# Optimization experiments

Hardware: AMD Instinct MI355X
Metric: run time of the kernel (lower is better)

Reference implementation:

```python
import jax, jax.numpy as jnp
import numpy as np

B, T, N, D, NH = 4, 12, 512, 512, 8
DH = D // NH
# Faithful quirk of the original: inside cal_attention, d = K.shape[-1] (the HEAD dim = 64)
# and it divides by sqrt(d / n_h) = sqrt(64/8) = sqrt(8), NOT sqrt(64).
SCALE = 1.0 / np.sqrt(DH / NH).astype(np.float32)
NEG = -1000000000.0


def setup_inputs() -> dict:
    key = jax.random.key(0)
    ks = jax.random.split(key, 9)
    s = 1.0 / np.sqrt(D).astype(np.float32)
    return {
        "V": jax.random.normal(ks[0], (B, T, N, D), jnp.float32),
        "K": jax.random.normal(ks[1], (B, T, N, D), jnp.float32),
        "Q": jax.random.normal(ks[2], (B, T, N, D), jnp.float32),
        "M": jax.random.randint(ks[3], (B, T, N, N), 0, 2, jnp.int32),
        "wx_w": jax.random.normal(ks[4], (3 * D, D), jnp.float32) * s,
        "wx_b": jax.random.normal(ks[5], (3 * D,), jnp.float32) * 0.02,
        "wo_w": jax.random.normal(ks[6], (D, D), jnp.float32) * s,
        "wo_b": jax.random.normal(ks[7], (D,), jnp.float32) * 0.02,
    }


def _split_heads(x):
    # [B,T,N,D] -> [B,T,h,N,d_h]
    b, t, n, _ = x.shape
    return x.reshape(b, t, n, NH, DH).transpose(0, 1, 3, 2, 4)


def reference(V, K, Q, M, wx_w, wx_b, wo_w, wo_b):
    # self-attention branch: Q, K, V all come from wx(Q); inputs V/K are ignored
    wx_o = Q @ wx_w.T + wx_b                      # [B,T,N,3D]
    q, k, v = jnp.split(wx_o, 3, axis=-1)
    q, k, v = _split_heads(q), _split_heads(k), _split_heads(v)  # [B,T,h,N,d_h]
    scores = jnp.einsum("bthqd,bthkd->bthqk", q, k) * SCALE      # [B,T,h,N,N]
    scores = scores + M[:, :, None, :, :].astype(scores.dtype) * NEG
    attn = jax.nn.softmax(scores, axis=-1)
    out = jnp.einsum("bthqk,bthkd->bthqd", attn, v)              # [B,T,h,N,d_h]
    out = out.transpose(0, 1, 3, 2, 4).reshape(B, T, N, D)       # concat heads
    return out @ wo_w.T + wo_b
```

## Files before the change

kernel.cpp:

```cpp
#include <hip/hip_runtime.h>
#include <cstdint>
#include <cstddef>

typedef __bf16 bf16x8_t __attribute__((ext_vector_type(8)));
typedef float f32x4_t __attribute__((ext_vector_type(4)));

#define SCALE 0.3535533905932738f
#define LOG2E 1.4426950408889634f
#define NEG -1000000000.0f

__device__ __forceinline__ unsigned short f2b(float f) {
    unsigned int u = __builtin_bit_cast(unsigned int, f);
    u += 0x7FFFu + ((u >> 16) & 1u);
    return (unsigned short)(u >> 16);
}

__device__ __forceinline__ int swz(int row, int chunk) {
    return row * 64 + (((chunk ^ (row & 7)) << 3));
}

__device__ __forceinline__ void gld16(const void* g, void* l) {
    __builtin_amdgcn_global_load_lds(
        (const __attribute__((address_space(1))) unsigned int*)g,
        (__attribute__((address_space(3))) unsigned int*)l,
        16, 0, 0);
}

__device__ __forceinline__ unsigned int cvt_pk_bf16(float lo, float hi) {
    unsigned int r;
    asm("v_cvt_pk_bf16_f32 %0, %1, %2" : "=v"(r) : "v"(lo), "v"(hi));
    return r;
}

__global__ __launch_bounds__(256) void cvt_kernel(const float* __restrict__ in,
                                                  unsigned short* __restrict__ out,
                                                  int n4) {
    int i = blockIdx.x * 256 + threadIdx.x;
    if (i >= n4) return;
    const float4 f = reinterpret_cast<const float4*>(in)[i];
    ushort4 o;
    o.x = f2b(f.x); o.y = f2b(f.y); o.z = f2b(f.z); o.w = f2b(f.w);
    reinterpret_cast<ushort4*>(out)[i] = o;
}

__global__ __launch_bounds__(256) void gemm_qkv(
    const unsigned short* __restrict__ A,
    const unsigned short* __restrict__ W,
    const float* __restrict__ bias,
    unsigned short* __restrict__ qb,
    unsigned short* __restrict__ kb,
    unsigned short* __restrict__ vT)
{
    __shared__ unsigned short As[128*64];
    __shared__ unsigned short Bs[128*64];
    const int tid = threadIdx.x;
    const int lane = tid & 63;
    const int l15 = lane & 15, lhi = lane >> 4;
    const int wid = tid >> 6, wr = wid >> 1, wc = wid & 1;
    const int bid = blockIdx.x;
    const int sid = (bid & 7) * 288 + (bid >> 3);
    const int m0 = (sid / 12) * 128, n0 = (sid % 12) * 128;
    const int rA = lane >> 3;
    const int sc = (lane & 7) ^ rA;

    f32x4_t acc[4][4] = {};

    for (int k0 = 0; k0 < 512; k0 += 64) {
        __syncthreads();
#pragma unroll
        for (int j = 0; j < 4; ++j) {
            const int ch = 4*wid + j;
            const int gr = ch*8 + rA;
            gld16(&A[(size_t)(m0+gr)*512 + k0 + sc*8], &As[ch*512]);
            gld16(&W[(size_t)(n0+gr)*512 + k0 + sc*8], &Bs[ch*512]);
        }
        asm volatile("s_waitcnt vmcnt(0)" ::: "memory");
        __syncthreads();
#pragma unroll
        for (int kk = 0; kk < 2; ++kk) {
            bf16x8_t af[4], bfr[4];
#pragma unroll
            for (int x = 0; x < 4; ++x) {
                af[x]  = *reinterpret_cast<const bf16x8_t*>(&As[swz(wr*64 + x*16 + l15, kk*4 + lhi)]);
                bfr[x] = *reinterpret_cast<const bf16x8_t*>(&Bs[swz(wc*64 + x*16 + l15, kk*4 + lhi)]);
            }
#pragma unroll
            for (int mi = 0; mi < 4; ++mi)
#pragma unroll
                for (int nj = 0; nj < 4; ++nj)
                    acc[mi][nj] = __builtin_amdgcn_mfma_f32_16x16x32_bf16(af[mi], bfr[nj], acc[mi][nj], 0, 0, 0);
        }
    }

#pragma unroll
    for (int mi = 0; mi < 4; ++mi) {
#pragma unroll
        for (int nj = 0; nj < 4; ++nj) {
            const int gn = n0 + wc*64 + nj*16 + l15;
            const float bi = bias[gn];
            const int which = gn >> 9, hh = (gn >> 6) & 7, dh = gn & 63;
#pragma unroll
            for (int i = 0; i < 4; ++i) {
                const int gm = m0 + wr*64 + mi*16 + lhi*4 + i;
                const int bt = gm >> 9, row = gm & 511;
                const float v = acc[mi][nj][i] + bi;
                const size_t ho = (size_t)bt*8 + hh;
                if (which == 0)      qb[ho*(512*64) + (size_t)row*64 + dh] = f2b(v * (SCALE * LOG2E));
                else if (which == 1) kb[ho*(512*64) + (size_t)row*64 + dh] = f2b(v);
                else                 vT[ho*(64*512) + (size_t)dh*512 + row] = f2b(v);
            }
        }
    }
}

__global__ __launch_bounds__(512, 4) void attn_kernel(
    const unsigned short* __restrict__ qb,
    const unsigned short* __restrict__ kb,
    const unsigned short* __restrict__ vT,
    const int* __restrict__ Mm,
    unsigned short* __restrict__ ob)
{
    __shared__ unsigned short Ks[2][64*64];
    __shared__ unsigned short Vs[2][64*64];
    __shared__ unsigned short Ps[8][32*40];

    const int tid = threadIdx.x;
    const int lane = tid & 63;
    const int w = tid >> 6;
    const int l15 = lane & 15, lhi = lane >> 4;
    const int bid = blockIdx.x;
    const int sid = (bid & 7) * 96 + (bid >> 3);
    const int qt = sid & 1;
    const int h  = (sid >> 1) & 7;
    const int bt = sid >> 4;
    const int q0 = qt*256 + w*32;
    const size_t hoQK = ((size_t)bt*8 + h) * (512*64);
    const size_t hoV  = ((size_t)bt*8 + h) * (64*512);

    const int rA = lane >> 3;
    const int sc = (lane & 7) ^ rA;
    const int trK = w*8 + rA;

    bf16x8_t qf[2][2];
#pragma unroll
    for (int qmi = 0; qmi < 2; ++qmi)
#pragma unroll
        for (int kk = 0; kk < 2; ++kk)
            qf[qmi][kk] = *reinterpret_cast<const bf16x8_t*>(
                &qb[hoQK + (size_t)(q0 + qmi*16 + l15)*64 + kk*32 + lhi*8]);

    bf16x8_t ones;
    {
        uint4 u = {0x3F803F80u, 0x3F803F80u, 0x3F803F80u, 0x3F803F80u};
        ones = __builtin_bit_cast(bf16x8_t, u);
    }

    f32x4_t of[2][4] = {};
    f32x4_t ofl[2] = {};

    const size_t mrow0 = ((size_t)bt*512 + q0 + l15) * 512;

    gld16(&kb[hoQK + (size_t)trK*64 + sc*8],          &Ks[0][w*512]);
    gld16(&vT[hoV + (size_t)(w*8 + rA)*512 + sc*8],   &Vs[0][w*512]);

    for (int kbk = 0; kbk < 8; ++kbk) {
        const int cur = kbk & 1;
        if (kbk < 7) {
            const int t = kbk + 1, nb = cur ^ 1;
            gld16(&kb[hoQK + (size_t)(t*64 + trK)*64 + sc*8],        &Ks[nb][w*512]);
            gld16(&vT[hoV + (size_t)(w*8 + rA)*512 + t*64 + sc*8],   &Vs[nb][w*512]);
            asm volatile("s_waitcnt vmcnt(2)" ::: "memory");
        } else {
            asm volatile("s_waitcnt vmcnt(0)" ::: "memory");
        }
        __syncthreads();

        int4 mv[4][2];
#pragma unroll
        for (int knj = 0; knj < 4; ++knj)
#pragma unroll
            for (int qmi = 0; qmi < 2; ++qmi)
                mv[knj][qmi] = *reinterpret_cast<const int4*>(
                    &Mm[mrow0 + (size_t)(qmi*16)*512 + kbk*64 + knj*16 + lhi*4]);

        f32x4_t sa[4][2] = {};
#pragma unroll
        for (int kk = 0; kk < 2; ++kk) {
            bf16x8_t kf[4];
#pragma unroll
            for (int knj = 0; knj < 4; ++knj)
                kf[knj] = *reinterpret_cast<const bf16x8_t*>(&Ks[cur][swz(knj*16 + l15, kk*4 + lhi)]);
#pragma unroll
            for (int knj = 0; knj < 4; ++knj)
#pragma unroll
                for (int qmi = 0; qmi < 2; ++qmi)
                    sa[knj][qmi] = __builtin_amdgcn_mfma_f32_16x16x32_bf16(kf[knj], qf[qmi][kk], sa[knj][qmi], 0, 0, 0);
        }

#pragma unroll
        for (int knj = 0; knj < 4; ++knj)
#pragma unroll
            for (int qmi = 0; qmi < 2; ++qmi) {
                sa[knj][qmi][0] = exp2f(fmaf((float)mv[knj][qmi].x, NEG, sa[knj][qmi][0]));
                sa[knj][qmi][1] = exp2f(fmaf((float)mv[knj][qmi].y, NEG, sa[knj][qmi][1]));
                sa[knj][qmi][2] = exp2f(fmaf((float)mv[knj][qmi].z, NEG, sa[knj][qmi][2]));
                sa[knj][qmi][3] = exp2f(fmaf((float)mv[knj][qmi].w, NEG, sa[knj][qmi][3]));
            }

#pragma unroll
        for (int half = 0; half < 2; ++half) {
#pragma unroll
            for (int qmi = 0; qmi < 2; ++qmi)
#pragma unroll
                for (int knjh = 0; knjh < 2; ++knjh) {
                    const int knj = half*2 + knjh;
                    const unsigned int p01 = cvt_pk_bf16(sa[knj][qmi][0], sa[knj][qmi][1]);
                    const unsigned int p23 = cvt_pk_bf16(sa[knj][qmi][2], sa[knj][qmi][3]);
                    const int base = (qmi*16 + l15)*40 + knjh*16 + lhi*4;
                    *reinterpret_cast<unsigned int*>(&Ps[w][base])     = p01;
                    *reinterpret_cast<unsigned int*>(&Ps[w][base + 2]) = p23;
                }

            bf16x8_t pf[2];
#pragma unroll
            for (int qmi = 0; qmi < 2; ++qmi)
                pf[qmi] = *reinterpret_cast<const bf16x8_t*>(&Ps[w][(qmi*16 + l15)*40 + lhi*8]);

            bf16x8_t vf[4];
#pragma unroll
            for (int dj = 0; dj < 4; ++dj)
                vf[dj] = *reinterpret_cast<const bf16x8_t*>(&Vs[cur][swz(dj*16 + l15, half*4 + lhi)]);

#pragma unroll
            for (int qmi = 0; qmi < 2; ++qmi) {
                ofl[qmi] = __builtin_amdgcn_mfma_f32_16x16x32_bf16(pf[qmi], ones, ofl[qmi], 0, 0, 0);
#pragma unroll
                for (int dj = 0; dj < 4; ++dj)
                    of[qmi][dj] = __builtin_amdgcn_mfma_f32_16x16x32_bf16(pf[qmi], vf[dj], of[qmi][dj], 0, 0, 0);
            }
        }

        __syncthreads();
    }

#pragma unroll
    for (int qmi = 0; qmi < 2; ++qmi)
#pragma unroll
        for (int i = 0; i < 4; ++i) {
            const int qrow = q0 + qmi*16 + lhi*4 + i;
            const float inv = 1.f / ofl[qmi][i];
#pragma unroll
            for (int dj = 0; dj < 4; ++dj)
                ob[((size_t)bt*512 + qrow)*512 + h*64 + dj*16 + l15] = f2b(of[qmi][dj][i] * inv);
        }
}

__global__ __launch_bounds__(256) void gemm_out(
    const unsigned short* __restrict__ A,
    const unsigned short* __restrict__ W,
    const float* __restrict__ bias,
    float* __restrict__ out)
{
    __shared__ unsigned short As[128*64];
    __shared__ unsigned short Bs[128*64];
    const int tid = threadIdx.x;
    const int lane = tid & 63;
    const int l15 = lane & 15, lhi = lane >> 4;
    const int wid = tid >> 6, wr = wid >> 1, wc = wid & 1;
    const int bid = blockIdx.x;
    const int sid = (bid & 7) * 96 + (bid >> 3);
    const int m0 = (sid / 4) * 128, n0 = (sid % 4) * 128;
    const int rA = lane >> 3;
    const int sc = (lane & 7) ^ rA;

    f32x4_t acc[4][4] = {};

    for (int k0 = 0; k0 < 512; k0 += 64) {
        __syncthreads();
#pragma unroll
        for (int j = 0; j < 4; ++j) {
            const int ch = 4*wid + j;
            const int gr = ch*8 + rA;
            gld16(&A[(size_t)(m0+gr)*512 + k0 + sc*8], &As[ch*512]);
            gld16(&W[(size_t)(n0+gr)*512 + k0 + sc*8], &Bs[ch*512]);
        }
        asm volatile("s_waitcnt vmcnt(0)" ::: "memory");
        __syncthreads();
#pragma unroll
        for (int kk = 0; kk < 2; ++kk) {
            bf16x8_t af[4], bfr[4];
#pragma unroll
            for (int x = 0; x < 4; ++x) {
                af[x]  = *reinterpret_cast<const bf16x8_t*>(&As[swz(wr*64 + x*16 + l15, kk*4 + lhi)]);
                bfr[x] = *reinterpret_cast<const bf16x8_t*>(&Bs[swz(wc*64 + x*16 + l15, kk*4 + lhi)]);
            }
#pragma unroll
            for (int mi = 0; mi < 4; ++mi)
#pragma unroll
                for (int nj = 0; nj < 4; ++nj)
                    acc[mi][nj] = __builtin_amdgcn_mfma_f32_16x16x32_bf16(af[mi], bfr[nj], acc[mi][nj], 0, 0, 0);
        }
    }

#pragma unroll
    for (int mi = 0; mi < 4; ++mi) {
#pragma unroll
        for (int nj = 0; nj < 4; ++nj) {
            const int gn = n0 + wc*64 + nj*16 + l15;
            const float bi = bias[gn];
#pragma unroll
            for (int i = 0; i < 4; ++i) {
                const int gm = m0 + wr*64 + mi*16 + lhi*4 + i;
                out[(size_t)gm*512 + gn] = acc[mi][nj][i] + bi;
            }
        }
    }
}

extern "C" void kernel_launch(void* const* d_in, const int* in_sizes, int n_in,
                              void* d_out, int out_size, void* d_ws, size_t ws_size,
                              hipStream_t stream) {
    (void)in_sizes; (void)n_in; (void)out_size; (void)ws_size;
    const float* Qin = (const float*)d_in[2];
    const int*   Mm  = (const int*)d_in[3];
    const float* wxw = (const float*)d_in[4];
    const float* wxb = (const float*)d_in[5];
    const float* wow = (const float*)d_in[6];
    const float* wob = (const float*)d_in[7];
    float* out = (float*)d_out;

    char* ws = (char*)d_ws;
    const size_t SZ_A  = (size_t)24576*512*2;
    const size_t SZ_WX = (size_t)1536*512*2;
    const size_t SZ_WO = (size_t)512*512*2;
    const size_t SZ_H  = (size_t)48*8*512*64*2;

    unsigned short* Abf  = (unsigned short*)(ws);
    unsigned short* Wxb  = (unsigned short*)(ws + SZ_A);
    unsigned short* Wob  = (unsigned short*)(ws + SZ_A + SZ_WX);
    unsigned short* qb   = (unsigned short*)(ws + SZ_A + SZ_WX + SZ_WO);
    unsigned short* kbuf = (unsigned short*)(ws + SZ_A + SZ_WX + SZ_WO + SZ_H);
    unsigned short* vT   = (unsigned short*)(ws + SZ_A + SZ_WX + SZ_WO + 2*SZ_H);
    unsigned short* attn = Abf;

    cvt_kernel<<<(24576*512/4)/256, 256, 0, stream>>>(Qin, Abf, 24576*512/4);
    cvt_kernel<<<(1536*512/4)/256, 256, 0, stream>>>(wxw, Wxb, 1536*512/4);
    cvt_kernel<<<(512*512/4)/256, 256, 0, stream>>>(wow, Wob, 512*512/4);

    gemm_qkv<<<2304, 256, 0, stream>>>(Abf, Wxb, wxb, qb, kbuf, vT);
    attn_kernel<<<768, 512, 0, stream>>>(qb, kbuf, vT, Mm, attn);
    gemm_out<<<768, 256, 0, stream>>>(attn, Wob, wob, out);
}
```

Measured before the change: 211.4 us.

## Pack attention mask to bytes and prefetch mask tiles with K/V loads

Adds a pre-pass that converts the int32 mask to uint8 in workspace, so the attention kernel reads four times fewer mask bytes. Mask loads are double-buffered and issued one tile ahead alongside the K/V async loads. The change also raises wave priority around MFMA blocks and uses the raw exp2 intrinsic. The cost is a full extra read of the int32 mask plus a write of the packed copy on every call, and higher register pressure from the prefetched mask values.

```diff
diff --git a/kernel.cpp b/kernel.cpp
--- a/kernel.cpp
+++ b/kernel.cpp
@@ -41,6 +41,18 @@
     ushort4 o;
     o.x = f2b(f.x); o.y = f2b(f.y); o.z = f2b(f.z); o.w = f2b(f.w);
     reinterpret_cast<ushort4*>(out)[i] = o;
+}
+
+__global__ __launch_bounds__(256) void pack_kernel(const int* __restrict__ in,
+                                                   unsigned char* __restrict__ out,
+                                                   int n4) {
+    int i = blockIdx.x * 256 + threadIdx.x;
+    if (i >= n4) return;
+    const int4 v = reinterpret_cast<const int4*>(in)[i];
+    uchar4 o;
+    o.x = (unsigned char)v.x; o.y = (unsigned char)v.y;
+    o.z = (unsigned char)v.z; o.w = (unsigned char)v.w;
+    reinterpret_cast<uchar4*>(out)[i] = o;
 }
 
 __global__ __launch_bounds__(256) void gemm_qkv(
@@ -113,11 +125,13 @@
     }
 }
 
+template<bool PACKED>
 __global__ __launch_bounds__(512, 4) void attn_kernel(
     const unsigned short* __restrict__ qb,
     const unsigned short* __restrict__ kb,
     const unsigned short* __restrict__ vT,
-    const int* __restrict__ Mm,
+    const int* __restrict__ Mi,
+    const unsigned char* __restrict__ Mp,
     unsigned short* __restrict__ ob)
 {
     __shared__ unsigned short Ks[2][64*64];
@@ -160,28 +174,37 @@
 
     const size_t mrow0 = ((size_t)bt*512 + q0 + l15) * 512;
 
-    gld16(&kb[hoQK + (size_t)trK*64 + sc*8],          &Ks[0][w*512]);
-    gld16(&vT[hoV + (size_t)(w*8 + rA)*512 + sc*8],   &Vs[0][w*512]);
-
-    for (int kbk = 0; kbk < 8; ++kbk) {
-        const int cur = kbk & 1;
-        if (kbk < 7) {
-            const int t = kbk + 1, nb = cur ^ 1;
-            gld16(&kb[hoQK + (size_t)(t*64 + trK)*64 + sc*8],        &Ks[nb][w*512]);
-            gld16(&vT[hoV + (size_t)(w*8 + rA)*512 + t*64 + sc*8],   &Vs[nb][w*512]);
-            asm volatile("s_waitcnt vmcnt(2)" ::: "memory");
-        } else {
-            asm volatile("s_waitcnt vmcnt(0)" ::: "memory");
-        }
-        __syncthreads();
-
-        int4 mv[4][2];
-#pragma unroll
-        for (int knj = 0; knj < 4; ++knj)
-#pragma unroll
-            for (int qmi = 0; qmi < 2; ++qmi)
-                mv[knj][qmi] = *reinterpret_cast<const int4*>(
-                    &Mm[mrow0 + (size_t)(qmi*16)*512 + kbk*64 + knj*16 + lhi*4]);
+    unsigned int mp8[2][8];
+    int4         mi4[2][8];
+
+#define MLOAD(buf, t)                                                                  \
+    do {                                                                               \
+        _Pragma("unroll")                                                              \
+        for (int x = 0; x < 8; ++x) {                                                  \
+            const int knj_ = x >> 1, qmi_ = x & 1;                                     \
+            const size_t off_ = mrow0 + (size_t)(qmi_*16)*512 + (size_t)(t)*64         \
+                                + knj_*16 + lhi*4;                                     \
+            if (PACKED) mp8[buf][x] = *reinterpret_cast<const unsigned int*>(&Mp[off_]); \
+            else        mi4[buf][x] = *reinterpret_cast<const int4*>(&Mi[off_]);       \
+        }                                                                              \
+    } while (0)
+
+    gld16(&kb[hoQK + (size_t)trK*64 + sc*8],        &Ks[0][w*512]);
+    gld16(&vT[hoV + (size_t)(w*8 + rA)*512 + sc*8], &Vs[0][w*512]);
+    MLOAD(0, 0);
+    asm volatile("s_waitcnt vmcnt(0)" ::: "memory");
+    __syncthreads();
+
+#pragma unroll
+    for (int t = 0; t < 8; ++t) {
+        const int cur = t & 1;
+
+        if (t < 7) {
+            const int nb = cur ^ 1;
+            gld16(&kb[hoQK + (size_t)((t+1)*64 + trK)*64 + sc*8],        &Ks[nb][w*512]);
+            gld16(&vT[hoV + (size_t)(w*8 + rA)*512 + (t+1)*64 + sc*8],   &Vs[nb][w*512]);
+            MLOAD(nb, t + 1);
+        }
 
         f32x4_t sa[4][2] = {};
 #pragma unroll
@@ -190,21 +213,34 @@
 #pragma unroll
             for (int knj = 0; knj < 4; ++knj)
                 kf[knj] = *reinterpret_cast<const bf16x8_t*>(&Ks[cur][swz(knj*16 + l15, kk*4 + lhi)]);
+            __builtin_amdgcn_s_setprio(1);
 #pragma unroll
             for (int knj = 0; knj < 4; ++knj)
 #pragma unroll
                 for (int qmi = 0; qmi < 2; ++qmi)
                     sa[knj][qmi] = __builtin_amdgcn_mfma_f32_16x16x32_bf16(kf[knj], qf[qmi][kk], sa[knj][qmi], 0, 0, 0);
+            __builtin_amdgcn_s_setprio(0);
         }
 
 #pragma unroll
         for (int knj = 0; knj < 4; ++knj)
 #pragma unroll
             for (int qmi = 0; qmi < 2; ++qmi) {
-                sa[knj][qmi][0] = exp2f(fmaf((float)mv[knj][qmi].x, NEG, sa[knj][qmi][0]));
-                sa[knj][qmi][1] = exp2f(fmaf((float)mv[knj][qmi].y, NEG, sa[knj][qmi][1]));
-                sa[knj][qmi][2] = exp2f(fmaf((float)mv[knj][qmi].z, NEG, sa[knj][qmi][2]));
-                sa[knj][qmi][3] = exp2f(fmaf((float)mv[knj][qmi].w, NEG, sa[knj][qmi][3]));
+                float m0, m1, m2, m3;
+                if (PACKED) {
+                    const unsigned int mu = mp8[cur][knj*2 + qmi];
+                    m0 = (float)(mu & 0xffu);
+                    m1 = (float)((mu >> 8) & 0xffu);
+                    m2 = (float)((mu >> 16) & 0xffu);
+                    m3 = (float)(mu >> 24);
+                } else {
+                    const int4 v = mi4[cur][knj*2 + qmi];
+                    m0 = (float)v.x; m1 = (float)v.y; m2 = (float)v.z; m3 = (float)v.w;
+                }
+                sa[knj][qmi][0] = __builtin_amdgcn_exp2f(fmaf(m0, NEG, sa[knj][qmi][0]));
+                sa[knj][qmi][1] = __builtin_amdgcn_exp2f(fmaf(m1, NEG, sa[knj][qmi][1]));
+                sa[knj][qmi][2] = __builtin_amdgcn_exp2f(fmaf(m2, NEG, sa[knj][qmi][2]));
+                sa[knj][qmi][3] = __builtin_amdgcn_exp2f(fmaf(m3, NEG, sa[knj][qmi][3]));
             }
 
 #pragma unroll
@@ -231,6 +267,7 @@
             for (int dj = 0; dj < 4; ++dj)
                 vf[dj] = *reinterpret_cast<const bf16x8_t*>(&Vs[cur][swz(dj*16 + l15, half*4 + lhi)]);
 
+            __builtin_amdgcn_s_setprio(1);
 #pragma unroll
             for (int qmi = 0; qmi < 2; ++qmi) {
                 ofl[qmi] = __builtin_amdgcn_mfma_f32_16x16x32_bf16(pf[qmi], ones, ofl[qmi], 0, 0, 0);
@@ -238,10 +275,15 @@
                 for (int dj = 0; dj < 4; ++dj)
                     of[qmi][dj] = __builtin_amdgcn_mfma_f32_16x16x32_bf16(pf[qmi], vf[dj], of[qmi][dj], 0, 0, 0);
             }
-        }
-
-        __syncthreads();
-    }
+            __builtin_amdgcn_s_setprio(0);
+        }
+
+        if (t < 7) {
+            asm volatile("s_waitcnt vmcnt(0)" ::: "memory");
+            __syncthreads();
+        }
+    }
+#undef MLOAD
 
 #pragma unroll
     for (int qmi = 0; qmi < 2; ++qmi)
@@ -320,7 +362,7 @@
 extern "C" void kernel_launch(void* const* d_in, const int* in_sizes, int n_in,
                               void* d_out, int out_size, void* d_ws, size_t ws_size,
                               hipStream_t stream) {
-    (void)in_sizes; (void)n_in; (void)out_size; (void)ws_size;
+    (void)in_sizes; (void)n_in; (void)out_size;
     const float* Qin = (const float*)d_in[2];
     const int*   Mm  = (const int*)d_in[3];
     const float* wxw = (const float*)d_in[4];
@@ -334,6 +376,7 @@
     const size_t SZ_WX = (size_t)1536*512*2;
     const size_t SZ_WO = (size_t)512*512*2;
     const size_t SZ_H  = (size_t)48*8*512*64*2;
+    const size_t SZ_M  = (size_t)48*512*512;
 
     unsigned short* Abf  = (unsigned short*)(ws);
     unsigned short* Wxb  = (unsigned short*)(ws + SZ_A);
@@ -341,13 +384,21 @@
     unsigned short* qb   = (unsigned short*)(ws + SZ_A + SZ_WX + SZ_WO);
     unsigned short* kbuf = (unsigned short*)(ws + SZ_A + SZ_WX + SZ_WO + SZ_H);
     unsigned short* vT   = (unsigned short*)(ws + SZ_A + SZ_WX + SZ_WO + 2*SZ_H);
+    unsigned char*  Mp   = (unsigned char*)(ws + SZ_A + SZ_WX + SZ_WO + 3*SZ_H);
     unsigned short* attn = Abf;
+
+    const bool packed = ws_size >= (SZ_A + SZ_WX + SZ_WO + 3*SZ_H + SZ_M);
 
     cvt_kernel<<<(24576*512/4)/256, 256, 0, stream>>>(Qin, Abf, 24576*512/4);
     cvt_kernel<<<(1536*512/4)/256, 256, 0, stream>>>(wxw, Wxb, 1536*512/4);
     cvt_kernel<<<(512*512/4)/256, 256, 0, stream>>>(wow, Wob, 512*512/4);
+    if (packed)
+        pack_kernel<<<(48*512*512/4)/256, 256, 0, stream>>>(Mm, Mp, 48*512*512/4);
 
     gemm_qkv<<<2304, 256, 0, stream>>>(Abf, Wxb, wxb, qb, kbuf, vT);
-    attn_kernel<<<768, 512, 0, stream>>>(qb, kbuf, vT, Mm, attn);
+    if (packed)
+        attn_kernel<true><<<768, 512, 0, stream>>>(qb, kbuf, vT, Mm, Mp, attn);
+    else
+        attn_kernel<false><<<768, 512, 0, stream>>>(qb, kbuf, vT, Mm, Mp, attn);
     gemm_out<<<768, 256, 0, stream>>>(attn, Wob, wob, out);
 }
```

Result: slower. 244.9 us (+15.9%).

## Replace LDS round-trip for P with permlane swaps, add setprio, raise occupancy

Applied to the files above, without the earlier changes.

The softmax numerator tile P is now rearranged from the MFMA output layout into the MFMA A-operand layout in registers using v_permlane32/16 swaps, instead of being written to and re-read from per-wave LDS scratch. This removes the Ps shared buffer and its LDS traffic, lowering LDS use so the launch bound can request 6 blocks per CU instead of 4. MFMA sequences are also wrapped in s_setprio to favour matrix issue across waves. The risk is added register pressure under the tighter occupancy target, and a possible permutation-order mismatch if the lane mapping is wrong.

```diff
diff --git a/kernel.cpp b/kernel.cpp
--- a/kernel.cpp
+++ b/kernel.cpp
@@ -113,7 +113,7 @@
     }
 }
 
-__global__ __launch_bounds__(512, 4) void attn_kernel(
+__global__ __launch_bounds__(512, 6) void attn_kernel(
     const unsigned short* __restrict__ qb,
     const unsigned short* __restrict__ kb,
     const unsigned short* __restrict__ vT,
@@ -122,7 +122,6 @@
 {
     __shared__ unsigned short Ks[2][64*64];
     __shared__ unsigned short Vs[2][64*64];
-    __shared__ unsigned short Ps[8][32*40];
 
     const int tid = threadIdx.x;
     const int lane = tid & 63;
@@ -160,8 +159,8 @@
 
     const size_t mrow0 = ((size_t)bt*512 + q0 + l15) * 512;
 
-    gld16(&kb[hoQK + (size_t)trK*64 + sc*8],          &Ks[0][w*512]);
-    gld16(&vT[hoV + (size_t)(w*8 + rA)*512 + sc*8],   &Vs[0][w*512]);
+    gld16(&kb[hoQK + (size_t)trK*64 + sc*8],        &Ks[0][w*512]);
+    gld16(&vT[hoV + (size_t)(w*8 + rA)*512 + sc*8], &Vs[0][w*512]);
 
     for (int kbk = 0; kbk < 8; ++kbk) {
         const int cur = kbk & 1;
@@ -190,11 +189,13 @@
 #pragma unroll
             for (int knj = 0; knj < 4; ++knj)
                 kf[knj] = *reinterpret_cast<const bf16x8_t*>(&Ks[cur][swz(knj*16 + l15, kk*4 + lhi)]);
+            __builtin_amdgcn_s_setprio(1);
 #pragma unroll
             for (int knj = 0; knj < 4; ++knj)
 #pragma unroll
                 for (int qmi = 0; qmi < 2; ++qmi)
                     sa[knj][qmi] = __builtin_amdgcn_mfma_f32_16x16x32_bf16(kf[knj], qf[qmi][kk], sa[knj][qmi], 0, 0, 0);
+            __builtin_amdgcn_s_setprio(0);
         }
 
 #pragma unroll
@@ -207,37 +208,44 @@
                 sa[knj][qmi][3] = exp2f(fmaf((float)mv[knj][qmi].w, NEG, sa[knj][qmi][3]));
             }
 
+        bf16x8_t pf[2][2];
+#pragma unroll
+        for (int qmi = 0; qmi < 2; ++qmi) {
+            unsigned int Ap[4], Bp[4];
+#pragma unroll
+            for (int knj = 0; knj < 4; ++knj) {
+                Ap[knj] = cvt_pk_bf16(sa[knj][qmi][0], sa[knj][qmi][1]);
+                Bp[knj] = cvt_pk_bf16(sa[knj][qmi][2], sa[knj][qmi][3]);
+            }
+#pragma unroll
+            for (int kk = 0; kk < 2; ++kk) {
+                unsigned int x  = Ap[kk*2], y  = Ap[kk*2+1];
+                unsigned int xb = Bp[kk*2], yb = Bp[kk*2+1];
+                asm volatile("v_permlane32_swap_b32 %0, %1" : "+v"(x),  "+v"(y));
+                asm volatile("v_permlane16_swap_b32 %0, %1" : "+v"(x),  "+v"(y));
+                asm volatile("v_permlane32_swap_b32 %0, %1" : "+v"(xb), "+v"(yb));
+                asm volatile("v_permlane16_swap_b32 %0, %1" : "+v"(xb), "+v"(yb));
+                uint4 u = {x, xb, y, yb};
+                pf[qmi][kk] = __builtin_bit_cast(bf16x8_t, u);
+            }
+        }
+
 #pragma unroll
         for (int half = 0; half < 2; ++half) {
-#pragma unroll
-            for (int qmi = 0; qmi < 2; ++qmi)
-#pragma unroll
-                for (int knjh = 0; knjh < 2; ++knjh) {
-                    const int knj = half*2 + knjh;
-                    const unsigned int p01 = cvt_pk_bf16(sa[knj][qmi][0], sa[knj][qmi][1]);
-                    const unsigned int p23 = cvt_pk_bf16(sa[knj][qmi][2], sa[knj][qmi][3]);
-                    const int base = (qmi*16 + l15)*40 + knjh*16 + lhi*4;
-                    *reinterpret_cast<unsigned int*>(&Ps[w][base])     = p01;
-                    *reinterpret_cast<unsigned int*>(&Ps[w][base + 2]) = p23;
-                }
-
-            bf16x8_t pf[2];
-#pragma unroll
-            for (int qmi = 0; qmi < 2; ++qmi)
-                pf[qmi] = *reinterpret_cast<const bf16x8_t*>(&Ps[w][(qmi*16 + l15)*40 + lhi*8]);
-
             bf16x8_t vf[4];
 #pragma unroll
             for (int dj = 0; dj < 4; ++dj)
                 vf[dj] = *reinterpret_cast<const bf16x8_t*>(&Vs[cur][swz(dj*16 + l15, half*4 + lhi)]);
 
+            __builtin_amdgcn_s_setprio(1);
 #pragma unroll
             for (int qmi = 0; qmi < 2; ++qmi) {
-                ofl[qmi] = __builtin_amdgcn_mfma_f32_16x16x32_bf16(pf[qmi], ones, ofl[qmi], 0, 0, 0);
+                ofl[qmi] = __builtin_amdgcn_mfma_f32_16x16x32_bf16(pf[qmi][half], ones, ofl[qmi], 0, 0, 0);
 #pragma unroll
                 for (int dj = 0; dj < 4; ++dj)
-                    of[qmi][dj] = __builtin_amdgcn_mfma_f32_16x16x32_bf16(pf[qmi], vf[dj], of[qmi][dj], 0, 0, 0);
-            }
+                    of[qmi][dj] = __builtin_amdgcn_mfma_f32_16x16x32_bf16(pf[qmi][half], vf[dj], of[qmi][dj], 0, 0, 0);
+            }
+            __builtin_amdgcn_s_setprio(0);
         }
 
         __syncthreads();
```

Result: slower. 474.8 us (+124.6%).
